# Kernel optimization log

Measured on AMD Instinct MI355X. Metric: run time of the kernel, lower is better.

## Reference

```python
import jax, jax.numpy as jnp
import numpy as np

D_MODEL = 512
N_HEADS = 8
D_K = D_MODEL // N_HEADS  # 64
EPS = 1e-5


def setup_inputs() -> dict:
    key = jax.random.key(0)
    ks = jax.random.split(key, 16)
    s = 0.02
    B, T = 4, 2048
    return {
        "x": jax.random.normal(ks[0], (B, T, D_MODEL), dtype=jnp.float32),
        # per-head q/k/v projections stacked over heads: [H, d_model, d_k]
        "Wq": jax.random.normal(ks[1], (N_HEADS, D_MODEL, D_K), dtype=jnp.float32) * s,
        "bq": jnp.zeros((N_HEADS, D_K), dtype=jnp.float32),
        "Wk": jax.random.normal(ks[2], (N_HEADS, D_MODEL, D_K), dtype=jnp.float32) * s,
        "bk": jnp.zeros((N_HEADS, D_K), dtype=jnp.float32),
        "Wv": jax.random.normal(ks[3], (N_HEADS, D_MODEL, D_K), dtype=jnp.float32) * s,
        "bv": jnp.zeros((N_HEADS, D_K), dtype=jnp.float32),
        "Wp": jax.random.normal(ks[4], (D_MODEL, D_MODEL), dtype=jnp.float32) * s,
        "bp": jnp.zeros((D_MODEL,), dtype=jnp.float32),
        "W1": jax.random.normal(ks[5], (D_MODEL, 4 * D_MODEL), dtype=jnp.float32) * s,
        "b1": jnp.zeros((4 * D_MODEL,), dtype=jnp.float32),
        "W2": jax.random.normal(ks[6], (4 * D_MODEL, D_MODEL), dtype=jnp.float32) * s,
        "b2": jnp.zeros((D_MODEL,), dtype=jnp.float32),
        "g1": jnp.ones((D_MODEL,), dtype=jnp.float32),
        "be1": jnp.zeros((D_MODEL,), dtype=jnp.float32),
        "g2": jnp.ones((D_MODEL,), dtype=jnp.float32),
        "be2": jnp.zeros((D_MODEL,), dtype=jnp.float32),
    }


def _layer_norm(x, g, b):
    mu = jnp.mean(x, axis=-1, keepdims=True)
    var = jnp.var(x, axis=-1, keepdims=True)
    return (x - mu) * jax.lax.rsqrt(var + EPS) * g + b


def _block(x, Wq, bq, Wk, bk, Wv, bv, Wp, bp, W1, b1, W2, b2, g1, be1, g2, be2):
    B, T, _ = x.shape
    h = _layer_norm(x, g1, be1)
    # batched per-head projections: [B, H, T, d_k]
    q = jnp.einsum('btd,hdk->bhtk', h, Wq) + bq[:, None, :]
    k = jnp.einsum('btd,hdk->bhtk', h, Wk) + bk[:, None, :]
    v = jnp.einsum('btd,hdk->bhtk', h, Wv) + bv[:, None, :]
    scores = jnp.einsum('bhtk,bhsk->bhts', q, k)  # [B, H, T, T]
    causal = jnp.tril(jnp.ones((T, T), dtype=bool))
    # faithful to source: mask with -1e9 BEFORE dividing by sqrt(d_k)
    scores = jnp.where(causal, scores, jnp.float32(-1e9))
    attn = jax.nn.softmax(scores / jnp.float32(np.sqrt(D_K)), axis=-1)
    o = jnp.einsum('bhts,bhsk->bhtk', attn, v)  # [B, H, T, d_k]
    o = o.transpose(0, 2, 1, 3).reshape(B, T, D_MODEL)  # concat heads
    x = x + o @ Wp + bp
    h2 = _layer_norm(x, g2, be2)
    ff = jax.nn.relu(h2 @ W1 + b1) @ W2 + b2
    return x + ff


def reference(x, Wq, bq, Wk, bk, Wv, bv, Wp, bp, W1, b1, W2, b2, g1, be1, g2, be2):
    return _block(x, Wq, bq, Wk, bk, Wv, bv, Wp, bp, W1, b1, W2, b2, g1, be1, g2, be2)
```

## Files before the change

### kernel.cpp

```cpp
#include <hip/hip_runtime.h>
#include <hip/hip_bf16.h>
#include <math.h>

#define BATCH 4
#define SEQ   2048
#define DM    512
#define NH    8
#define DK    64
#define FF    2048
#define BT    (BATCH * SEQ)

#define SCALE_Q 0.18033688011112042f

typedef short bf16x8 __attribute__((ext_vector_type(8)));
typedef float f32x4  __attribute__((ext_vector_type(4)));

static __device__ inline short f2bf(float f) {
  union { float f; unsigned u; } v; v.f = f;
  unsigned r = (v.u + 0x7fffu + ((v.u >> 16) & 1u)) >> 16;
  return (short)r;
}

static __device__ __forceinline__ void gload16(const short* g, short* l) {
  __builtin_amdgcn_global_load_lds(
      (const __attribute__((address_space(1))) void*)g,
      (__attribute__((address_space(3))) void*)l, 16, 0, 0);
}

static __device__ __forceinline__ void xcd_swizzle(int& bx, int& by) {
  int gx = gridDim.x;
  int nwg = gx * gridDim.y;
  int id = blockIdx.x + gx * blockIdx.y;
  int nid = (id & 7) * (nwg >> 3) + (id >> 3);
  bx = nid % gx;
  by = nid / gx;
}

__global__ __launch_bounds__(256) void ln_kernel(
    const float* __restrict__ x, const float* __restrict__ gamma,
    const float* __restrict__ beta, short* __restrict__ out) {
  int row = blockIdx.x;
  const float* xr = x + (size_t)row * DM;
  int t = threadIdx.x;
  float v0 = xr[t], v1 = xr[t + 256];
  float s = v0 + v1;
  float sq = v0 * v0 + v1 * v1;
  for (int off = 32; off; off >>= 1) {
    s  += __shfl_xor(s, off);
    sq += __shfl_xor(sq, off);
  }
  __shared__ float ssum[4], ssq[4];
  int wave = t >> 6, lane = t & 63;
  if (lane == 0) { ssum[wave] = s; ssq[wave] = sq; }
  __syncthreads();
  if (t == 0) {
    float S = ssum[0] + ssum[1] + ssum[2] + ssum[3];
    float Q = ssq[0] + ssq[1] + ssq[2] + ssq[3];
    float mu = S * (1.0f / DM);
    float var = Q * (1.0f / DM) - mu * mu;
    ssum[0] = mu;
    ssq[0] = rsqrtf(var + 1e-5f);
  }
  __syncthreads();
  float mu = ssum[0], rstd = ssq[0];
  short* orow = out + (size_t)row * DM;
  orow[t]       = f2bf((v0 - mu) * rstd * gamma[t]       + beta[t]);
  orow[t + 256] = f2bf((v1 - mu) * rstd * gamma[t + 256] + beta[t + 256]);
}

__global__ __launch_bounds__(256) void wconv_kernel(
    const float* Wq, const float* Wk, const float* Wv,
    const float* Wp, const float* W1, const float* W2,
    short* wqkv, short* wpt, short* w1t, short* w2t) {
  int z = blockIdx.z;
  const float* src; short* dst; int R, C;
  if (z < 24) {
    int m = z >> 3, hh = z & 7;
    const float* s0 = (m == 0) ? Wq : (m == 1) ? Wk : Wv;
    src = s0 + (size_t)hh * 512 * 64;
    dst = wqkv + ((size_t)(m * 512 + hh * 64)) * 512;
    R = 512; C = 64;
  } else if (z == 24) { src = Wp; dst = wpt; R = 512;  C = 512;  }
  else if (z == 25)   { src = W1; dst = w1t; R = 512;  C = 2048; }
  else                { src = W2; dst = w2t; R = 2048; C = 512;  }
  int tx = blockIdx.x, ty = blockIdx.y;
  if (tx >= C / 64 || ty >= R / 64) return;
  __shared__ float Ts[64][68];
  int t = threadIdx.x;
  int r = t >> 2, c0 = (t & 3) * 16;
  const float* sp = src + (size_t)(ty * 64 + r) * C + tx * 64 + c0;
#pragma unroll
  for (int i = 0; i < 16; i += 4) {
    float4 v = *(const float4*)(sp + i);
    Ts[c0 + i + 0][r] = v.x; Ts[c0 + i + 1][r] = v.y;
    Ts[c0 + i + 2][r] = v.z; Ts[c0 + i + 3][r] = v.w;
  }
  __syncthreads();
  short* dp = dst + (size_t)(tx * 64 + r) * R + ty * 64 + c0;
  short tmp[16];
#pragma unroll
  for (int i = 0; i < 16; ++i) tmp[i] = f2bf(Ts[r][c0 + i]);
  *(int4*)(dp)     = *(int4*)&tmp[0];
  *(int4*)(dp + 8) = *(int4*)&tmp[8];
}

template<int TM, int TN>
__device__ __forceinline__ void gemm_core(
    const short* __restrict__ A, const short* __restrict__ Bw,
    int m0, int n0, int K, short* smem, f32x4 (&acc)[TM / 32][TN / 32]) {
  constexpr int AF = TM / 32, BF = TN / 32;
  constexpr int AC = TM / 64, BC = TN / 64;
  constexpr int BUFS = (TM + TN) * 32;
  int t = threadIdx.x;
  int wave = t >> 6, lane = t & 63, quad = lane >> 4, l16 = lane & 15;
  int wr = wave >> 1, wc = wave & 1;

  size_t aoff[AC], boff[BC];
  int aldsoff[AC], bldsoff[BC];
#pragma unroll
  for (int c = 0; c < AC; ++c) {
    int p = c * 256 + t, row = p >> 2, lg = (p & 3) ^ ((row >> 1) & 3);
    aoff[c] = (size_t)(m0 + row) * K + lg * 8;
    aldsoff[c] = c * 2048 + wave * 512;
  }
#pragma unroll
  for (int c = 0; c < BC; ++c) {
    int p = c * 256 + t, row = p >> 2, lg = (p & 3) ^ ((row >> 1) & 3);
    boff[c] = (size_t)(n0 + row) * K + lg * 8;
    bldsoff[c] = TM * 32 + c * 2048 + wave * 512;
  }

#pragma unroll
  for (int c = 0; c < AC; ++c) gload16(A + aoff[c], smem + aldsoff[c]);
#pragma unroll
  for (int c = 0; c < BC; ++c) gload16(Bw + boff[c], smem + bldsoff[c]);

  int physo = (quad ^ ((l16 >> 1) & 3)) * 8;

  for (int k0 = 0; k0 < K; k0 += 32) {
    short* cbuf = smem + ((k0 >> 5) & 1) * BUFS;
    __syncthreads();
    if (k0 + 32 < K) {
      short* nbuf = smem + (((k0 >> 5) & 1) ^ 1) * BUFS;
#pragma unroll
      for (int c = 0; c < AC; ++c) gload16(A + aoff[c] + k0 + 32, nbuf + aldsoff[c]);
#pragma unroll
      for (int c = 0; c < BC; ++c) gload16(Bw + boff[c] + k0 + 32, nbuf + bldsoff[c]);
    }
    bf16x8 af[AF], bfr[BF];
#pragma unroll
    for (int i = 0; i < AF; ++i)
      af[i] = *(const bf16x8*)&cbuf[(wr * (TM / 2) + i * 16 + l16) * 32 + physo];
#pragma unroll
    for (int j = 0; j < BF; ++j)
      bfr[j] = *(const bf16x8*)&cbuf[TM * 32 + (wc * (TN / 2) + j * 16 + l16) * 32 + physo];
#pragma unroll
    for (int i = 0; i < AF; ++i)
#pragma unroll
      for (int j = 0; j < BF; ++j)
        acc[i][j] = __builtin_amdgcn_mfma_f32_16x16x32_bf16(bfr[j], af[i], acc[i][j], 0, 0, 0);
  }
}

template<int TM, int TN>
__global__ __launch_bounds__(256) void mgemm_kernel(
    const short* __restrict__ A, const short* __restrict__ Bw,
    const float* __restrict__ bias, const float* __restrict__ res,
    void* __restrict__ C, int N, int K, int dorelu, int bf16out) {
  __shared__ __align__(16) short smem[(TM + TN) * 64];
  f32x4 acc[TM / 32][TN / 32];
  f32x4 zf = {0.f, 0.f, 0.f, 0.f};
#pragma unroll
  for (int i = 0; i < TM / 32; ++i)
#pragma unroll
    for (int j = 0; j < TN / 32; ++j) acc[i][j] = zf;
  int bx, by;
  xcd_swizzle(bx, by);
  int m0 = by * TM, n0 = bx * TN;
  gemm_core<TM, TN>(A, Bw, m0, n0, K, smem, acc);

  int t = threadIdx.x;
  int wave = t >> 6, lane = t & 63, quad = lane >> 4, l16 = lane & 15;
  int wr = wave >> 1, wc = wave & 1;
#pragma unroll
  for (int i = 0; i < TM / 32; ++i) {
    int m = m0 + wr * (TM / 2) + i * 16 + l16;
#pragma unroll
    for (int j = 0; j < TN / 32; ++j) {
      int nb = n0 + wc * (TN / 2) + j * 16 + quad * 4;
      float4 bv = *(const float4*)&bias[nb];
      float v[4] = {acc[i][j][0] + bv.x, acc[i][j][1] + bv.y,
                    acc[i][j][2] + bv.z, acc[i][j][3] + bv.w};
      if (dorelu) {
#pragma unroll
        for (int r = 0; r < 4; ++r) v[r] = fmaxf(v[r], 0.0f);
      }
      size_t off = (size_t)m * N + nb;
      if (res) {
        float4 rv = *(const float4*)(res + off);
        v[0] += rv.x; v[1] += rv.y; v[2] += rv.z; v[3] += rv.w;
      }
      if (bf16out) {
        short tmp[4] = {f2bf(v[0]), f2bf(v[1]), f2bf(v[2]), f2bf(v[3])};
        *(int2*)((short*)C + off) = *(int2*)tmp;
      } else {
        float4 outv = {v[0], v[1], v[2], v[3]};
        *(float4*)((float*)C + off) = outv;
      }
    }
  }
}

__global__ __launch_bounds__(256) void qkv_kernel(
    const short* __restrict__ A, const short* __restrict__ Bw,
    const float* __restrict__ bq, const float* __restrict__ bk,
    const float* __restrict__ bv,
    short* __restrict__ q, short* __restrict__ k, short* __restrict__ vt) {
  __shared__ __align__(16) short smem[17408];
  f32x4 acc[4][4];
  f32x4 zf = {0.f, 0.f, 0.f, 0.f};
#pragma unroll
  for (int i = 0; i < 4; ++i)
#pragma unroll
    for (int j = 0; j < 4; ++j) acc[i][j] = zf;
  int bx, by;
  xcd_swizzle(bx, by);
  int m0 = by * 128, n0 = bx * 128;
  gemm_core<128, 128>(A, Bw, m0, n0, DM, smem, acc);

  int t = threadIdx.x;
  int wave = t >> 6, lane = t & 63, quad = lane >> 4, l16 = lane & 15;
  int wr = wave >> 1, wc = wave & 1;

  if (n0 < 1024) {
    short* out = (n0 < 512) ? q : k;
    const float* bias = (n0 < 512) ? bq + n0 : bk + (n0 - 512);
    float scale = (n0 < 512) ? SCALE_Q : 1.0f;
    int ncol0 = (n0 < 512) ? n0 : n0 - 512;
#pragma unroll
    for (int i = 0; i < 4; ++i) {
      int m = m0 + wr * 64 + i * 16 + l16;
#pragma unroll
      for (int j = 0; j < 4; ++j) {
        int nb = wc * 64 + j * 16 + quad * 4;
        float4 bvv = *(const float4*)&bias[nb];
        short tmp[4];
        tmp[0] = f2bf((acc[i][j][0] + bvv.x) * scale);
        tmp[1] = f2bf((acc[i][j][1] + bvv.y) * scale);
        tmp[2] = f2bf((acc[i][j][2] + bvv.z) * scale);
        tmp[3] = f2bf((acc[i][j][3] + bvv.w) * scale);
        *(int2*)(out + (size_t)m * DM + ncol0 + nb) = *(int2*)tmp;
      }
    }
  } else {
    const float* bias = bv + (n0 - 1024);
    __syncthreads();
    short* Ts = smem;
#pragma unroll
    for (int i = 0; i < 4; ++i) {
      int ml = wr * 64 + i * 16 + l16;
#pragma unroll
      for (int j = 0; j < 4; ++j) {
        int nb = wc * 64 + j * 16 + quad * 4;
        float4 bvv = *(const float4*)&bias[nb];
        Ts[(nb + 0) * 136 + ml] = f2bf(acc[i][j][0] + bvv.x);
        Ts[(nb + 1) * 136 + ml] = f2bf(acc[i][j][1] + bvv.y);
        Ts[(nb + 2) * 136 + ml] = f2bf(acc[i][j][2] + bvv.z);
        Ts[(nb + 3) * 136 + ml] = f2bf(acc[i][j][3] + bvv.w);
      }
    }
    __syncthreads();
    int nl = t >> 1, half = (t & 1) * 64;
    int gn = (n0 - 1024) + nl;
    int hh = gn >> 6, dk = gn & 63;
    int bidx = m0 >> 11, s0 = (m0 & 2047) + half;
    short* dst = vt + ((size_t)((bidx * NH + hh) * DK + dk)) * SEQ + s0;
    const short* srcT = &Ts[nl * 136 + half];
#pragma unroll
    for (int i2 = 0; i2 < 64; i2 += 8)
      *(int4*)(dst + i2) = *(const int4*)(srcT + i2);
  }
}

template<bool DIAG>
static __device__ __forceinline__ void attn_tile(
    const short* __restrict__ KsC, const short* __restrict__ VsC,
    short* __restrict__ Psw, const bf16x8& qf0, const bf16x8& qf1,
    f32x4 (&o_acc)[4], float& l_part, int quad, int l16,
    int keyb0, int qrow) {
  f32x4 zf = {0.f, 0.f, 0.f, 0.f};
  int sw = l16 & 7;

#pragma unroll
  for (int nt = 0; nt < 4; ++nt) {
    int krow = nt * 16 + l16;
    bf16x8 ka0 = *(const bf16x8*)&KsC[krow * 64 + ((quad ^ sw) * 8)];
    bf16x8 ka1 = *(const bf16x8*)&KsC[krow * 64 + (((4 + quad) ^ sw) * 8)];
    f32x4 s = __builtin_amdgcn_mfma_f32_16x16x32_bf16(ka0, qf0, zf, 0, 0, 0);
    s = __builtin_amdgcn_mfma_f32_16x16x32_bf16(ka1, qf1, s, 0, 0, 0);
    int keyb = keyb0 + nt * 16 + quad * 4;
    float pr[4];
#pragma unroll
    for (int r = 0; r < 4; ++r) {
      float e = exp2f(s[r]);
      pr[r] = (DIAG && (keyb + r > qrow)) ? 0.0f : e;
      l_part += pr[r];
    }
    unsigned pk0 = __builtin_amdgcn_perm(
        __float_as_uint(pr[1]), __float_as_uint(pr[0]), 0x07060302u);
    unsigned pk1 = __builtin_amdgcn_perm(
        __float_as_uint(pr[3]), __float_as_uint(pr[2]), 0x07060302u);
    int2 w = {(int)pk0, (int)pk1};
    *(int2*)&Psw[l16 * 64 + (((nt * 2 + (quad >> 1)) ^ sw) << 3) +
                 ((quad & 1) * 4)] = w;
  }

  bf16x8 apf0 = *(const bf16x8*)&Psw[l16 * 64 + ((quad ^ sw) * 8)];
  bf16x8 apf1 = *(const bf16x8*)&Psw[l16 * 64 + (((4 + quad) ^ sw) * 8)];
  __builtin_amdgcn_s_setprio(1);
#pragma unroll
  for (int nt2 = 0; nt2 < 4; ++nt2) {
    int vrow = nt2 * 16 + l16;
    bf16x8 vf0 = *(const bf16x8*)&VsC[vrow * 64 + ((quad ^ sw) * 8)];
    bf16x8 vf1 = *(const bf16x8*)&VsC[vrow * 64 + (((4 + quad) ^ sw) * 8)];
    o_acc[nt2] = __builtin_amdgcn_mfma_f32_16x16x32_bf16(vf0, apf0, o_acc[nt2], 0, 0, 0);
    o_acc[nt2] = __builtin_amdgcn_mfma_f32_16x16x32_bf16(vf1, apf1, o_acc[nt2], 0, 0, 0);
  }
  __builtin_amdgcn_s_setprio(0);
}

__global__ __launch_bounds__(256) void fattn_kernel(
    const short* __restrict__ Q, const short* __restrict__ Kg,
    const short* __restrict__ Vt, short* __restrict__ O) {
  int id = blockIdx.x + 32 * (blockIdx.y + NH * blockIdx.z);
  int c = id & 7, j = id >> 3;
  int g = c * 4 + (j & 3);
  int qt = 31 - (j >> 2);
  int h = g & 7, b = g >> 3;
  int q0 = qt * 64;
  int t = threadIdx.x, wave = t >> 6, lane = t & 63, quad = lane >> 4, l16 = lane & 15;

  __shared__ __align__(16) short Ks[2][64 * 64];
  __shared__ __align__(16) short Vs[2][64 * 64];
  __shared__ __align__(16) short Ps[4][16 * 64];

  f32x4 zf = {0.f, 0.f, 0.f, 0.f};
  const short* qp = Q + ((size_t)(b * SEQ + q0 + wave * 16 + l16)) * DM + h * DK;
  bf16x8 qf0 = *(const bf16x8*)(qp + quad * 8);
  bf16x8 qf1 = *(const bf16x8*)(qp + 32 + quad * 8);

  f32x4 o_acc[4];
  float l_part = 0.0f;
#pragma unroll
  for (int i = 0; i < 4; ++i) o_acc[i] = zf;

  const short* kb = Kg + ((size_t)(b * SEQ)) * DM + h * DK;
  const short* vb = Vt + ((size_t)((b * NH + h) * DK)) * SEQ;

  int row0 = t >> 3,         lg0 = (t & 7) ^ (row0 & 7);
  int row1 = (256 + t) >> 3, lg1 = ((256 + t) & 7) ^ (row1 & 7);
  const short* kp0 = kb + (size_t)row0 * DM + lg0 * 8;
  const short* kp1 = kb + (size_t)row1 * DM + lg1 * 8;
  const short* vp0 = vb + (size_t)row0 * SEQ + lg0 * 8;
  const short* vp1 = vb + (size_t)row1 * SEQ + lg1 * 8;
  int lo0 = wave * 512, lo1 = 2048 + wave * 512;

#define STAGE_KV(B) do {                                     \
    gload16(kp0, &Ks[B][lo0]); gload16(kp1, &Ks[B][lo1]);    \
    gload16(vp0, &Vs[B][lo0]); gload16(vp1, &Vs[B][lo1]);    \
    kp0 += 64 * DM; kp1 += 64 * DM; vp0 += 64; vp1 += 64; } while (0)

  STAGE_KV(0);

  int qrow = q0 + wave * 16 + l16;
  short* Psw = &Ps[wave][0];

  int buf = 0;
  for (int kt = 0; kt < qt; ++kt) {
    __syncthreads();
    STAGE_KV(buf ^ 1);
    attn_tile<false>(&Ks[buf][0], &Vs[buf][0], Psw, qf0, qf1,
                     o_acc, l_part, quad, l16, 0, qrow);
    buf ^= 1;
  }
  __syncthreads();
  attn_tile<true>(&Ks[buf][0], &Vs[buf][0], Psw, qf0, qf1,
                  o_acc, l_part, quad, l16, qt * 64, qrow);

  float lf = l_part;
  lf += __shfl_xor(lf, 16);
  lf += __shfl_xor(lf, 32);
  float inv = 1.0f / lf;
  short* orow = O + ((size_t)(b * SEQ) + qrow) * DM + h * DK;
#pragma unroll
  for (int nt2 = 0; nt2 < 4; ++nt2) {
    short tmp[4];
#pragma unroll
    for (int r = 0; r < 4; ++r) tmp[r] = f2bf(o_acc[nt2][r] * inv);
    *(int2*)(orow + nt2 * 16 + quad * 4) = *(int2*)tmp;
  }
#undef STAGE_KV
}

extern "C" void kernel_launch(void* const* d_in, const int* in_sizes, int n_in,
                              void* d_out, int out_size, void* d_ws, size_t ws_size,
                              hipStream_t stream) {
  const float* x   = (const float*)d_in[0];
  const float* Wq  = (const float*)d_in[1];
  const float* bq  = (const float*)d_in[2];
  const float* Wk  = (const float*)d_in[3];
  const float* bk  = (const float*)d_in[4];
  const float* Wv  = (const float*)d_in[5];
  const float* bv  = (const float*)d_in[6];
  const float* Wp  = (const float*)d_in[7];
  const float* bp  = (const float*)d_in[8];
  const float* W1  = (const float*)d_in[9];
  const float* b1  = (const float*)d_in[10];
  const float* W2  = (const float*)d_in[11];
  const float* b2  = (const float*)d_in[12];
  const float* g1  = (const float*)d_in[13];
  const float* be1 = (const float*)d_in[14];
  const float* g2  = (const float*)d_in[15];
  const float* be2 = (const float*)d_in[16];
  float* out = (float*)d_out;

  char* wsb = (char*)d_ws;
  const size_t SB = (size_t)BT * DM * 2;
  short* h    = (short*)(wsb);
  short* q    = (short*)(wsb + SB);
  short* k    = (short*)(wsb + 2 * SB);
  short* vt   = (short*)(wsb + 3 * SB);
  short* o    = (short*)(wsb + 4 * SB);
  float* x2   = (float*)(wsb + 5 * SB);
  short* h2   = (short*)(wsb + 5 * SB + (size_t)BT * DM * 4);
  short* ff   = (short*)(wsb + 6 * SB + (size_t)BT * DM * 4);
  short* wqkv = (short*)(wsb + 6 * SB + (size_t)BT * DM * 4 + (size_t)BT * FF * 2);
  short* wpt  = wqkv + 1536 * 512;
  short* w1t  = wpt + 512 * 512;
  short* w2t  = w1t + 2048 * 512;

  dim3 blk(256);

  wconv_kernel<<<dim3(32, 32, 27), blk, 0, stream>>>(Wq, Wk, Wv, Wp, W1, W2,
                                                     wqkv, wpt, w1t, w2t);
  ln_kernel<<<BT, blk, 0, stream>>>(x, g1, be1, h);

  qkv_kernel<<<dim3(12, 64), blk, 0, stream>>>(h, wqkv, bq, bk, bv, q, k, vt);

  fattn_kernel<<<dim3(32, NH, BATCH), blk, 0, stream>>>(q, k, vt, o);

  mgemm_kernel<64, 64><<<dim3(8, 128), blk, 0, stream>>>(o, wpt, bp, x, x2, DM, DM, 0, 0);
  ln_kernel<<<BT, blk, 0, stream>>>(x2, g2, be2, h2);
  mgemm_kernel<128, 128><<<dim3(16, 64), blk, 0, stream>>>(h2, w1t, b1, nullptr, ff, FF, DM, 1, 1);
  mgemm_kernel<64, 64><<<dim3(8, 128), blk, 0, stream>>>(ff, w2t, b2, x2, out, DM, FF, 0, 0);
}
```

Before: 266.2 us.

## Double flash-attention query tile to 128 rows with 8 waves sharing K/V loads

The attention kernel now processes 128 query rows per block using 512 threads (8 waves), so each staged 64-row K/V tile is reused by twice as many waves. Each thread issues one K and one V global-to-LDS load per tile instead of two, and the last two key tiles run with causal masking. The grid becomes a 1D launch of 512 blocks, ordered so that long and short query tiles alternate for load balance. In exchange there are half as many blocks, each with more threads, which changes occupancy, and some waves compute fully masked work on the diagonal tiles.

```diff
diff --git a/kernel.cpp b/kernel.cpp
--- a/kernel.cpp
+++ b/kernel.cpp
@@ -329,23 +329,26 @@
   __builtin_amdgcn_s_setprio(0);
 }
 
-__global__ __launch_bounds__(256) void fattn_kernel(
+__global__ __launch_bounds__(512) void fattn_kernel(
     const short* __restrict__ Q, const short* __restrict__ Kg,
     const short* __restrict__ Vt, short* __restrict__ O) {
-  int id = blockIdx.x + 32 * (blockIdx.y + NH * blockIdx.z);
+  int id = blockIdx.x;
   int c = id & 7, j = id >> 3;
-  int g = c * 4 + (j & 3);
-  int qt = 31 - (j >> 2);
+  int jj = (j < 32) ? j : (j - 32);
+  int g = c * 4 + (jj & 3);
+  int qts = (j < 32) ? (15 - (jj >> 2)) : (jj >> 2);
   int h = g & 7, b = g >> 3;
-  int q0 = qt * 64;
+  int q0 = qts * 128;
+  int NT = 2 * qts + 2;
   int t = threadIdx.x, wave = t >> 6, lane = t & 63, quad = lane >> 4, l16 = lane & 15;
 
   __shared__ __align__(16) short Ks[2][64 * 64];
   __shared__ __align__(16) short Vs[2][64 * 64];
-  __shared__ __align__(16) short Ps[4][16 * 64];
+  __shared__ __align__(16) short Ps[8][16 * 64];
 
   f32x4 zf = {0.f, 0.f, 0.f, 0.f};
-  const short* qp = Q + ((size_t)(b * SEQ + q0 + wave * 16 + l16)) * DM + h * DK;
+  int qrow = q0 + wave * 16 + l16;
+  const short* qp = Q + ((size_t)(b * SEQ + qrow)) * DM + h * DK;
   bf16x8 qf0 = *(const bf16x8*)(qp + quad * 8);
   bf16x8 qf1 = *(const bf16x8*)(qp + 32 + quad * 8);
 
@@ -357,26 +360,21 @@
   const short* kb = Kg + ((size_t)(b * SEQ)) * DM + h * DK;
   const short* vb = Vt + ((size_t)((b * NH + h) * DK)) * SEQ;
 
-  int row0 = t >> 3,         lg0 = (t & 7) ^ (row0 & 7);
-  int row1 = (256 + t) >> 3, lg1 = ((256 + t) & 7) ^ (row1 & 7);
-  const short* kp0 = kb + (size_t)row0 * DM + lg0 * 8;
-  const short* kp1 = kb + (size_t)row1 * DM + lg1 * 8;
-  const short* vp0 = vb + (size_t)row0 * SEQ + lg0 * 8;
-  const short* vp1 = vb + (size_t)row1 * SEQ + lg1 * 8;
-  int lo0 = wave * 512, lo1 = 2048 + wave * 512;
-
-#define STAGE_KV(B) do {                                     \
-    gload16(kp0, &Ks[B][lo0]); gload16(kp1, &Ks[B][lo1]);    \
-    gload16(vp0, &Vs[B][lo0]); gload16(vp1, &Vs[B][lo1]);    \
-    kp0 += 64 * DM; kp1 += 64 * DM; vp0 += 64; vp1 += 64; } while (0)
+  int row = t >> 3, lg = (t & 7) ^ (row & 7);
+  const short* kp = kb + (size_t)row * DM + lg * 8;
+  const short* vp = vb + (size_t)row * SEQ + lg * 8;
+  int wlo = wave * 512;
+
+#define STAGE_KV(B) do {                         \
+    gload16(kp, &Ks[B][wlo]);                    \
+    gload16(vp, &Vs[B][wlo]);                    \
+    kp += 64 * DM; vp += 64; } while (0)
 
   STAGE_KV(0);
 
-  int qrow = q0 + wave * 16 + l16;
   short* Psw = &Ps[wave][0];
-
   int buf = 0;
-  for (int kt = 0; kt < qt; ++kt) {
+  for (int kt = 0; kt < NT - 2; ++kt) {
     __syncthreads();
     STAGE_KV(buf ^ 1);
     attn_tile<false>(&Ks[buf][0], &Vs[buf][0], Psw, qf0, qf1,
@@ -384,8 +382,13 @@
     buf ^= 1;
   }
   __syncthreads();
+  STAGE_KV(buf ^ 1);
   attn_tile<true>(&Ks[buf][0], &Vs[buf][0], Psw, qf0, qf1,
-                  o_acc, l_part, quad, l16, qt * 64, qrow);
+                  o_acc, l_part, quad, l16, (NT - 2) * 64, qrow);
+  buf ^= 1;
+  __syncthreads();
+  attn_tile<true>(&Ks[buf][0], &Vs[buf][0], Psw, qf0, qf1,
+                  o_acc, l_part, quad, l16, (NT - 1) * 64, qrow);
 
   float lf = l_part;
   lf += __shfl_xor(lf, 16);
@@ -447,7 +450,7 @@
 
   qkv_kernel<<<dim3(12, 64), blk, 0, stream>>>(h, wqkv, bq, bk, bv, q, k, vt);
 
-  fattn_kernel<<<dim3(32, NH, BATCH), blk, 0, stream>>>(q, k, vt, o);
+  fattn_kernel<<<dim3(512), dim3(512), 0, stream>>>(q, k, vt, o);
 
   mgemm_kernel<64, 64><<<dim3(8, 128), blk, 0, stream>>>(o, wpt, bp, x, x2, DM, DM, 0, 0);
   ln_kernel<<<BT, blk, 0, stream>>>(x2, g2, be2, h2);
```

After: 268.7 us. Within noise of the previous version (+0.9%).
